# Kernel tuning notes

Hardware: AMD Instinct MI355X
Metric: run time of the kernel (lower is better)

Reference implementation:

```python
import jax, jax.numpy as jnp
import numpy as np

NS, NF, D = 50000, 100000, 128
E1, E2 = 600000, 600000


def setup_inputs() -> dict:
    key = jax.random.key(0)
    ks = jax.random.split(key, 9)
    return {
        "h_station": jax.random.normal(ks[0], (NS, D), dtype=jnp.float32),
        "h_feature": jax.random.normal(ks[1], (NF, D), dtype=jnp.float32),
        "Wself": jax.random.normal(ks[2], (3, 2, D, D), dtype=jnp.float32) * (1.0 / np.sqrt(D)),
        "Wneigh": jax.random.normal(ks[3], (3, 2, D, D), dtype=jnp.float32) * (1.0 / np.sqrt(D)),
        "bias": jnp.zeros((3, 2, D), dtype=jnp.float32),
        "hf_src": jax.random.randint(ks[4], (E1,), 0, NF, dtype=jnp.int32),
        "hf_dst": jax.random.randint(ks[5], (E1,), 0, NS, dtype=jnp.int32),
        "tt_src": jax.random.randint(ks[6], (E2,), 0, NS, dtype=jnp.int32),
        "tt_dst": jax.random.randint(ks[7], (E2,), 0, NS, dtype=jnp.int32),
    }


def _mean_agg(h_src, src, dst, n_dst):
    # gather source features along edges, segment-mean into destinations
    msgs = h_src[src]  # [E, D]
    s = jax.ops.segment_sum(msgs, dst, num_segments=n_dst)
    deg = jax.ops.segment_sum(jnp.ones((src.shape[0], 1), h_src.dtype), dst, num_segments=n_dst)
    return s / jnp.maximum(deg, 1.0)  # zero-in-degree nodes -> 0 (DGL behavior)


def _sage(h_dst, neigh, Ws, Wn, b):
    # DGL SAGEConv (mean): act(fc_self(h_dst) + fc_neigh(neigh) + bias)
    return jax.nn.relu(h_dst @ Ws + neigh @ Wn + b)


def reference(h_station, h_feature, Wself, Wneigh, bias, hf_src, hf_dst, tt_src, tt_dst):
    ns = h_station.shape[0]
    # --- layer 1: HeteroGraphConv aggregate='sum' over both relations (dst='station')
    n_hf = _mean_agg(h_feature, hf_src, hf_dst, ns)
    n_tt = _mean_agg(h_station, tt_src, tt_dst, ns)
    out_hf = _sage(h_station, n_hf, Wself[0, 0], Wneigh[0, 0], bias[0, 0])
    out_tt = _sage(h_station, n_tt, Wself[0, 1], Wneigh[0, 1], bias[0, 1])
    h = out_hf + out_tt
    # --- layers 2,3: 'feature' repr no longer present -> HAS_FEATURE relation skipped
    for l in (1, 2):
        n_tt = _mean_agg(h, tt_src, tt_dst, ns)
        h = _sage(h, n_tt, Wself[l, 1], Wneigh[l, 1], bias[l, 1])
    return h
```

## Files before the change

kernel.cpp:

```cpp
#include <hip/hip_runtime.h>

#define D 128
#define NBIN 256
#define K1_EPB 4096
#define BCAP 6144

typedef __attribute__((ext_vector_type(8)))  short s16x8;
typedef __attribute__((ext_vector_type(4)))  short s16x4;
typedef __attribute__((ext_vector_type(16))) float f32x16;

static __device__ __forceinline__ unsigned short f2bf(float x) {
    unsigned u = __builtin_bit_cast(unsigned, x);
    unsigned r = (u + 0x7FFF + ((u >> 16) & 1)) >> 16;
    return (unsigned short)r;
}
static __device__ __forceinline__ float bf2f(unsigned short h) {
    unsigned u = ((unsigned)h) << 16;
    return __builtin_bit_cast(float, u);
}
static __device__ __forceinline__ float bflo(unsigned v) {
    return __builtin_bit_cast(float, v << 16);
}
static __device__ __forceinline__ float bfhi(unsigned v) {
    return __builtin_bit_cast(float, v & 0xFFFF0000u);
}


__global__ __launch_bounds__(256) void convert_kernel(
    const float* __restrict__ h_station, unsigned short* __restrict__ st_h,
    int ns_elem, int nbs,
    const float* __restrict__ h_feature, unsigned short* __restrict__ feat_h,
    int nf_elem, int nbf,
    const float* __restrict__ Wself, const float* __restrict__ Wneigh,
    short* __restrict__ wt)
{
    int b = blockIdx.x;
    int tid = threadIdx.x;
    if (b < nbs) {
        int i = (b * 256 + tid) * 4;
        if (i < ns_elem) {
            float4 v = *(const float4*)(h_station + i);
            s16x4 hv;
            hv[0] = (short)f2bf(v.x);
            hv[1] = (short)f2bf(v.y);
            hv[2] = (short)f2bf(v.z);
            hv[3] = (short)f2bf(v.w);
            *(s16x4*)(st_h + i) = hv;
        }
        return;
    }
    b -= nbs;
    if (b < nbf) {
        int i = (b * 256 + tid) * 4;
        if (i < nf_elem) {
            float4 v = *(const float4*)(h_feature + i);
            s16x4 hv;
            hv[0] = (short)f2bf(v.x);
            hv[1] = (short)f2bf(v.y);
            hv[2] = (short)f2bf(v.z);
            hv[3] = (short)f2bf(v.w);
            *(s16x4*)(feat_h + i) = hv;
        }
        return;
    }
    b -= nbf;
    {
        int g = b * 256 + tid;
        int m = g >> 11;
        int e = g & 2047;
        int n  = e >> 4;
        int kg = e & 15;
        int kk0 = kg >> 3;
        int kl0 = (kg & 7) * 8;
        int pair = m >> 1, s = m & 1;
        int l = (pair == 3) ? 2 : ((pair == 2) ? 1 : 0);
        int r = (pair == 0) ? 0 : 1;
        const float* W = (s ? Wneigh : Wself) + (size_t)(l * 2 + r) * D * D;
        s16x8 hv;
        #pragma unroll
        for (int c = 0; c < 8; ++c) {
            int k = kk0 * 64 + kl0 + c;
            hv[c] = (short)f2bf(W[(size_t)k * D + n]);
        }
        int ksb = kl0 ^ ((n & 7) << 3);
        size_t base = ((size_t)(pair * 2 + s) * 2 + kk0) * 8192;
        *(s16x8*)&wt[base + n * 64 + ksb] = hv;
    }
}


__global__ __launch_bounds__(256) void hist_rank_kernel(
    const int* __restrict__ dst1, int E1, int nblk1, int* __restrict__ hist1,
    unsigned short* __restrict__ rank1,
    const int* __restrict__ dst2, int E2, int nblk2, int* __restrict__ hist2,
    unsigned short* __restrict__ rank2)
{
    __shared__ int h[NBIN];
    int b = blockIdx.x;
    const int* dst; int E, nblk; int* hist; unsigned short* rank;
    if (b < nblk1) { dst = dst1; E = E1; nblk = nblk1; hist = hist1; rank = rank1; }
    else { b -= nblk1; dst = dst2; E = E2; nblk = nblk2; hist = hist2; rank = rank2; }
    int t = threadIdx.x;
    h[t] = 0;
    __syncthreads();
    int base = b * K1_EPB;
    #pragma unroll 1
    for (int j = 0; j < 16; ++j) {
        int i = base + j * 256 + t;
        if (i < E) {
            int bin = dst[i] >> 8;
            int r = atomicAdd(&h[bin], 1);
            rank[i] = (unsigned short)r;
        }
    }
    __syncthreads();
    hist[t * nblk + b] = h[t];
}

__global__ __launch_bounds__(256) void scan_blocks_g(
    const int* __restrict__ in1, int* __restrict__ out1, int* __restrict__ bs1, int L1,
    const int* __restrict__ in2, int* __restrict__ out2, int* __restrict__ bs2, int L2,
    int nb1)
{
    int gid = blockIdx.x;
    const int* in; int* out; int* bs; int b; int L;
    if (gid < nb1) { in = in1; out = out1; bs = bs1; b = gid; L = L1; }
    else          { in = in2; out = out2; bs = bs2; b = gid - nb1; L = L2; }
    int t = threadIdx.x;
    int i0 = b * 1024 + t * 4;
    int4 v = make_int4(0, 0, 0, 0);
    if (i0 + 3 < L) v = *(const int4*)(in + i0);
    else {
        if (i0 + 0 < L) v.x = in[i0 + 0];
        if (i0 + 1 < L) v.y = in[i0 + 1];
        if (i0 + 2 < L) v.z = in[i0 + 2];
        if (i0 + 3 < L) v.w = in[i0 + 3];
    }
    __shared__ int sm[256];
    sm[t] = v.x + v.y + v.z + v.w;
    __syncthreads();
    for (int off = 1; off < 256; off <<= 1) {
        int x = (t >= off) ? sm[t - off] : 0;
        __syncthreads();
        sm[t] += x;
        __syncthreads();
    }
    int excl = (t > 0) ? sm[t - 1] : 0;
    if (i0 + 0 < L) out[i0 + 0] = excl;
    if (i0 + 1 < L) out[i0 + 1] = excl + v.x;
    if (i0 + 2 < L) out[i0 + 2] = excl + v.x + v.y;
    if (i0 + 3 < L) out[i0 + 3] = excl + v.x + v.y + v.z;
    if (t == 255) bs[b] = sm[255];
}

__global__ __launch_bounds__(256) void scan_offsets_g(
    int* __restrict__ out1, const int* __restrict__ bs1, int L1,
    int* __restrict__ out2, const int* __restrict__ bs2, int L2, int nb1)
{
    int gid = blockIdx.x;
    int* out; const int* bs; int b; int L;
    if (gid < nb1) { out = out1; bs = bs1; b = gid; L = L1; }
    else          { out = out2; bs = bs2; b = gid - nb1; L = L2; }
    int t = threadIdx.x;
    int lane = t & 63;
    int partial = 0;
    for (int i = lane; i < b; i += 64) partial += bs[i];
    #pragma unroll
    for (int off = 32; off; off >>= 1) partial += __shfl_xor(partial, off);
    if (partial == 0) return;
    int i0 = b * 1024 + t * 4;
    if (i0 + 0 < L) out[i0 + 0] += partial;
    if (i0 + 1 < L) out[i0 + 1] += partial;
    if (i0 + 2 < L) out[i0 + 2] += partial;
    if (i0 + 3 < L) out[i0 + 3] += partial;
}

__global__ __launch_bounds__(256) void scatter_kernel(
    const int* __restrict__ dst1, const int* __restrict__ src1,
    const unsigned short* __restrict__ rank1, const int* __restrict__ off1,
    unsigned* __restrict__ bkt1, int E1, int nblk1,
    const int* __restrict__ dst2, const int* __restrict__ src2,
    const unsigned short* __restrict__ rank2, const int* __restrict__ off2,
    unsigned* __restrict__ bkt2, int E2, int nblk2)
{
    int b = blockIdx.x;
    const int* dst; const int* src; const unsigned short* rank; const int* off;
    unsigned* bkt; int E, nblk;
    if (b < nblk1) { dst = dst1; src = src1; rank = rank1; off = off1; bkt = bkt1; E = E1; nblk = nblk1; }
    else { b -= nblk1; dst = dst2; src = src2; rank = rank2; off = off2; bkt = bkt2; E = E2; nblk = nblk2; }
    int t = threadIdx.x;
    int base = b * K1_EPB;
    #pragma unroll 1
    for (int j = 0; j < 16; ++j) {
        int i = base + j * 256 + t;
        if (i < E) {
            int d = dst[i];
            int bin = d >> 8;
            int pos = off[bin * nblk + b] + rank[i];
            bkt[pos] = ((unsigned)(d & 255) << 24) | (unsigned)src[i];
        }
    }
}

__global__ __launch_bounds__(256) void bucket_csr_kernel(
    const unsigned* __restrict__ bkt1, const int* __restrict__ off1, int E1, int nblk1,
    int* __restrict__ col1, int* __restrict__ rp1,
    const unsigned* __restrict__ bkt2, const int* __restrict__ off2, int E2, int nblk2,
    int* __restrict__ col2, int* __restrict__ rp2, int NSn)
{
    __shared__ int h[NBIN];
    __shared__ int pre[NBIN];
    __shared__ int cur[NBIN];
    __shared__ int colbuf[BCAP];
    int bin = blockIdx.x;
    const unsigned* bkt; const int* off; int E, nblk; int* col; int* rp;
    if (bin < NBIN) { bkt = bkt1; off = off1; E = E1; nblk = nblk1; col = col1; rp = rp1; }
    else { bin -= NBIN; bkt = bkt2; off = off2; E = E2; nblk = nblk2; col = col2; rp = rp2; }
    int t = threadIdx.x;
    int start = off[bin * nblk];
    int end = (bin == NBIN - 1) ? E : off[(bin + 1) * nblk];
    int n = end - start;

    h[t] = 0;
    __syncthreads();
    for (int p = t; p < n; p += 256) atomicAdd(&h[bkt[start + p] >> 24], 1);
    __syncthreads();
    int hv = h[t];
    pre[t] = hv;
    __syncthreads();
    for (int o = 1; o < 256; o <<= 1) {
        int x = (t >= o) ? pre[t - o] : 0;
        __syncthreads();
        pre[t] += x;
        __syncthreads();
    }
    int excl = pre[t] - hv;
    cur[t] = excl;
    __syncthreads();
    for (int p = t; p < n; p += 256) {
        unsigned v = bkt[start + p];
        int lo = v >> 24;
        int pos = atomicAdd(&cur[lo], 1);
        if (pos < BCAP) colbuf[pos] = (int)(v & 0xFFFFFF);
    }
    __syncthreads();
    for (int p = t; p < n; p += 256) col[start + p] = colbuf[p];
    int dstid = bin * 256 + t;
    if (dstid < NSn) rp[dstid] = start + excl;
    if (bin == 0 && t == 0) rp[NSn] = E;
}


static __device__ __forceinline__ void agg_body(
    const unsigned short* __restrict__ hsrc, const int* __restrict__ rowptr,
    const int* __restrict__ col, unsigned short* __restrict__ oh,
    int row4, int ndst, int lane)
{
    const int q  = lane >> 4;
    const int ql = lane & 15;
    const int row = row4 + q;
    const bool valid = row < ndst;
    int beg = 0, end = 0;
    if (valid) { beg = rowptr[row]; end = rowptr[row + 1]; }
    int deg = end - beg;

    float a0 = 0.f, a1 = 0.f, a2 = 0.f, a3 = 0.f;
    float a4 = 0.f, a5 = 0.f, a6 = 0.f, a7 = 0.f;
    const unsigned short* base = hsrc + ql * 8;

    for (int b = beg; b < end; b += 16) {
        int n = min(16, end - b);
        int myidx = (ql < n) ? col[b + ql] : 0;
        int j = 0;
        for (; j + 2 <= n; j += 2) {
            int s0 = __shfl(myidx, (q << 4) + j);
            int s1 = __shfl(myidx, (q << 4) + j + 1);
            uint4 v0 = *(const uint4*)(base + (size_t)s0 * D);
            uint4 v1 = *(const uint4*)(base + (size_t)s1 * D);
            a0 += bflo(v0.x); a1 += bfhi(v0.x);
            a2 += bflo(v0.y); a3 += bfhi(v0.y);
            a4 += bflo(v0.z); a5 += bfhi(v0.z);
            a6 += bflo(v0.w); a7 += bfhi(v0.w);
            a0 += bflo(v1.x); a1 += bfhi(v1.x);
            a2 += bflo(v1.y); a3 += bfhi(v1.y);
            a4 += bflo(v1.z); a5 += bfhi(v1.z);
            a6 += bflo(v1.w); a7 += bfhi(v1.w);
        }
        if (j < n) {
            int s0 = __shfl(myidx, (q << 4) + j);
            uint4 v0 = *(const uint4*)(base + (size_t)s0 * D);
            a0 += bflo(v0.x); a1 += bfhi(v0.x);
            a2 += bflo(v0.y); a3 += bfhi(v0.y);
            a4 += bflo(v0.z); a5 += bfhi(v0.z);
            a6 += bflo(v0.w); a7 += bfhi(v0.w);
        }
    }
    if (valid) {
        float inv = 1.0f / fmaxf((float)deg, 1.0f);
        s16x8 o;
        o[0] = (short)f2bf(a0 * inv);
        o[1] = (short)f2bf(a1 * inv);
        o[2] = (short)f2bf(a2 * inv);
        o[3] = (short)f2bf(a3 * inv);
        o[4] = (short)f2bf(a4 * inv);
        o[5] = (short)f2bf(a5 * inv);
        o[6] = (short)f2bf(a6 * inv);
        o[7] = (short)f2bf(a7 * inv);
        *(s16x8*)(oh + (size_t)row * D + ql * 8) = o;
    }
}

__global__ __launch_bounds__(256) void agg_mean_kernel(
    const unsigned short* __restrict__ hsrc, const int* __restrict__ rowptr,
    const int* __restrict__ col, unsigned short* __restrict__ oh, int ndst) {
    int wave = (blockIdx.x * blockDim.x + threadIdx.x) >> 6;
    int row4 = wave * 4;
    if (row4 >= ndst) return;
    agg_body(hsrc, rowptr, col, oh, row4, ndst, threadIdx.x & 63);
}

__global__ __launch_bounds__(256) void agg_l1_kernel(
    const unsigned short* __restrict__ feat, const int* __restrict__ rp_hf,
    const int* __restrict__ col_hf, unsigned short* __restrict__ n1,
    const unsigned short* __restrict__ st, const int* __restrict__ rp_tt,
    const int* __restrict__ col_tt, unsigned short* __restrict__ n2,
    int ndst, int gsplit)
{
    int b = blockIdx.x;
    if (b < gsplit) {
        int row4 = ((b * 256 + threadIdx.x) >> 6) * 4;
        if (row4 >= ndst) return;
        agg_body(feat, rp_hf, col_hf, n1, row4, ndst, threadIdx.x & 63);
    } else {
        int row4 = (((b - gsplit) * 256 + threadIdx.x) >> 6) * 4;
        if (row4 >= ndst) return;
        agg_body(st, rp_tt, col_tt, n2, row4, ndst, threadIdx.x & 63);
    }
}


template<bool ACC, bool WF32>
__global__ __launch_bounds__(256) void sage_gemm_kernel(
    const unsigned short* __restrict__ Ah_g, const unsigned short* __restrict__ Nh_g,
    const short* __restrict__ wtp, const float* __restrict__ bias,
    float* __restrict__ Yf, unsigned short* __restrict__ Yh, int M)
{
    __shared__ short lds[16384];
    short* AhS = lds;
    short* BhS = lds + 4096;

    const int tid = threadIdx.x;
    const int l = tid & 63, w = tid >> 6;
    const int wr = w >> 1, wc = w & 1;
    const int row0 = blockIdx.x * 64;

    f32x16 acc[2] = {};

    const int s_row = tid >> 2;
    const int s_k   = (tid & 3) * 16;
    const int s_sw  = (s_row & 7) << 3;
    const int arow  = wr * 32 + (l & 31);
    const int fsw   = (l & 7) << 3;
    const int afk   = (l >> 5) * 8;

    #pragma unroll 1
    for (int st = 0; st < 4; ++st) {
        const unsigned short* Hg = (st < 2) ? Ah_g : Nh_g;
        const unsigned short* hrow = Hg + (size_t)(row0 + s_row) * D + (st & 1) * 64 + s_k;
        s16x8 a0 = *(const s16x8*)(hrow);
        s16x8 a1 = *(const s16x8*)(hrow + 8);
        const short* wsrc = wtp + (size_t)st * 8192;
        s16x8 b0 = *(const s16x8*)(wsrc + tid * 8);
        s16x8 b1 = *(const s16x8*)(wsrc + 2048 + tid * 8);
        s16x8 b2 = *(const s16x8*)(wsrc + 4096 + tid * 8);
        s16x8 b3 = *(const s16x8*)(wsrc + 6144 + tid * 8);
        __syncthreads();
        *(s16x8*)&AhS[s_row * 64 + (s_k ^ s_sw)]       = a0;
        *(s16x8*)&AhS[s_row * 64 + ((s_k + 8) ^ s_sw)] = a1;
        *(s16x8*)&BhS[tid * 8]        = b0;
        *(s16x8*)&BhS[2048 + tid * 8] = b1;
        *(s16x8*)&BhS[4096 + tid * 8] = b2;
        *(s16x8*)&BhS[6144 + tid * 8] = b3;
        __syncthreads();
        #pragma unroll
        for (int kc = 0; kc < 4; ++kc) {
            int ak = (kc * 16 + afk) ^ fsw;
            s16x8 ah = *(const s16x8*)&AhS[arow * 64 + ak];
            #pragma unroll
            for (int nt = 0; nt < 2; ++nt) {
                int brow = wc * 64 + nt * 32 + (l & 31);
                s16x8 bh = *(const s16x8*)&BhS[brow * 64 + ak];
                acc[nt] = __builtin_amdgcn_mfma_f32_32x32x16_bf16(ah, bh, acc[nt], 0, 0, 0);
            }
        }
    }

    __syncthreads();
    float* fstage = (float*)lds;
    const int colb = l & 31;
    const int rq4  = (l >> 5) * 4;
    #pragma unroll
    for (int nt = 0; nt < 2; ++nt) {
        int col = wc * 64 + nt * 32 + colb;
        float bias_c = bias[col];
        #pragma unroll
        for (int g = 0; g < 4; ++g) {
            #pragma unroll
            for (int q = 0; q < 4; ++q) {
                int r = wr * 32 + q + g * 8 + rq4;
                fstage[r * 128 + col] = fmaxf(acc[nt][g * 4 + q] + bias_c, 0.f);
            }
        }
    }
    __syncthreads();
    int orow = tid >> 2;
    int ocol = (tid & 3) * 32;
    int grow = row0 + orow;
    if (grow < M) {
        size_t base = (size_t)grow * D + ocol;
        float vals[32];
        #pragma unroll
        for (int c = 0; c < 32; c += 4)
            *(float4*)&vals[c] = *(const float4*)&fstage[orow * 128 + ocol + c];
        if (ACC) {
            #pragma unroll
            for (int c8 = 0; c8 < 4; ++c8) {
                s16x8 oh = *(const s16x8*)(Yh + base + c8 * 8);
                #pragma unroll
                for (int e = 0; e < 8; ++e)
                    vals[c8 * 8 + e] += bf2f((unsigned short)oh[e]);
            }
        }
        if (WF32) {
            #pragma unroll
            for (int c = 0; c < 32; c += 4)
                *(float4*)(Yf + base + c) = *(const float4*)&vals[c];
        } else {
            #pragma unroll
            for (int c8 = 0; c8 < 4; ++c8) {
                s16x8 hv;
                #pragma unroll
                for (int e = 0; e < 8; ++e)
                    hv[e] = (short)f2bf(vals[c8 * 8 + e]);
                *(s16x8*)(Yh + base + c8 * 8) = hv;
            }
        }
    }
}


extern "C" void kernel_launch(void* const* d_in, const int* in_sizes, int n_in,
                              void* d_out, int out_size, void* d_ws, size_t ws_size,
                              hipStream_t stream) {
    const float* h_station = (const float*)d_in[0];
    const float* h_feature = (const float*)d_in[1];
    const float* Wself     = (const float*)d_in[2];
    const float* Wneigh    = (const float*)d_in[3];
    const float* bias      = (const float*)d_in[4];
    const int* hf_src = (const int*)d_in[5];
    const int* hf_dst = (const int*)d_in[6];
    const int* tt_src = (const int*)d_in[7];
    const int* tt_dst = (const int*)d_in[8];

    const int NS = in_sizes[0] / D;
    const int NF = in_sizes[1] / D;
    const int E1 = in_sizes[5];
    const int E2 = in_sizes[7];
    const int NSP = (NS + 63) & ~63;

    char* ws = (char*)d_ws;
    size_t off = 0;
    auto alloc = [&](size_t bytes) -> void* {
        void* p = ws + off;
        off = (off + bytes + 255) & ~(size_t)255;
        return p;
    };
    unsigned short* st_h  = (unsigned short*)alloc((size_t)NSP * D * 2);
    unsigned short* n_h   = (unsigned short*)alloc((size_t)NSP * D * 2);
    unsigned short* n_h2  = (unsigned short*)alloc((size_t)NSP * D * 2);
    unsigned short* hbreg = (unsigned short*)alloc((size_t)2 * NSP * D * 2);
    unsigned short* hb_h  = hbreg;
    int* rp_hf    = (int*)alloc((size_t)(NS + 1) * sizeof(int));
    int* col_hf   = (int*)alloc((size_t)E1 * sizeof(int));
    int* rp_tt    = (int*)alloc((size_t)(NS + 1) * sizeof(int));
    int* col_tt   = (int*)alloc((size_t)E2 * sizeof(int));
    short* wt     = (short*)alloc((size_t)4 * 32768 * sizeof(short));

    const int nblk1 = (E1 + K1_EPB - 1) / K1_EPB;
    const int nblk2 = (E2 + K1_EPB - 1) / K1_EPB;
    const int L1 = NBIN * nblk1;
    const int L2 = NBIN * nblk2;
    int* hist1 = (int*)alloc((size_t)L1 * sizeof(int));
    int* hist2 = (int*)alloc((size_t)L2 * sizeof(int));
    int* off1  = (int*)alloc((size_t)L1 * sizeof(int));
    int* off2  = (int*)alloc((size_t)L2 * sizeof(int));
    unsigned short* rank1 = (unsigned short*)alloc((size_t)E1 * 2);
    unsigned short* rank2 = (unsigned short*)alloc((size_t)E2 * 2);
    unsigned* bkt1 = (unsigned*)alloc((size_t)E1 * sizeof(unsigned));
    unsigned* bkt2 = (unsigned*)alloc((size_t)E2 * sizeof(unsigned));
    const int nbs1 = (L1 + 1023) / 1024;
    const int nbs2 = (L2 + 1023) / 1024;
    int* bsA = (int*)alloc((size_t)nbs1 * sizeof(int));
    int* bsB = (int*)alloc((size_t)nbs2 * sizeof(int));

    unsigned short* feat_h = hbreg;

    const int tpb = 256;
    int nbs = (NS * D / 4 + tpb - 1) / tpb;
    int nbf = (NF * D / 4 + tpb - 1) / tpb;

    convert_kernel<<<nbs + nbf + 64, tpb, 0, stream>>>(
        h_station, st_h, NS * D, nbs, h_feature, feat_h, NF * D, nbf,
        Wself, Wneigh, wt);
    hist_rank_kernel<<<nblk1 + nblk2, tpb, 0, stream>>>(
        hf_dst, E1, nblk1, hist1, rank1, tt_dst, E2, nblk2, hist2, rank2);
    scan_blocks_g<<<nbs1 + nbs2, tpb, 0, stream>>>(
        hist1, off1, bsA, L1, hist2, off2, bsB, L2, nbs1);
    scan_offsets_g<<<nbs1 + nbs2, tpb, 0, stream>>>(
        off1, bsA, L1, off2, bsB, L2, nbs1);
    scatter_kernel<<<nblk1 + nblk2, tpb, 0, stream>>>(
        hf_dst, hf_src, rank1, off1, bkt1, E1, nblk1,
        tt_dst, tt_src, rank2, off2, bkt2, E2, nblk2);
    bucket_csr_kernel<<<2 * NBIN, tpb, 0, stream>>>(
        bkt1, off1, E1, nblk1, col_hf, rp_hf,
        bkt2, off2, E2, nblk2, col_tt, rp_tt, NS);

    int gagg  = (NS + 15) / 16;
    int ggemm = NSP / 64;

    auto BI = [&](int lidx, int r) { return bias + (size_t)(lidx * 2 + r) * D; };
    auto WT = [&](int pair) { return wt + (size_t)pair * 32768; };

    float* out = (float*)d_out;

    agg_l1_kernel<<<2 * gagg, tpb, 0, stream>>>(feat_h, rp_hf, col_hf, n_h,
                                                st_h, rp_tt, col_tt, n_h2, NS, gagg);
    sage_gemm_kernel<false, false><<<ggemm, tpb, 0, stream>>>(
        st_h, n_h, WT(0), BI(0,0), nullptr, hb_h, NS);
    sage_gemm_kernel<true, false><<<ggemm, tpb, 0, stream>>>(
        st_h, n_h2, WT(1), BI(0,1), nullptr, hb_h, NS);

    agg_mean_kernel<<<gagg, tpb, 0, stream>>>(hb_h, rp_tt, col_tt, n_h, NS);
    sage_gemm_kernel<false, false><<<ggemm, tpb, 0, stream>>>(
        hb_h, n_h, WT(2), BI(1,1), nullptr, hb_h, NS);

    agg_mean_kernel<<<gagg, tpb, 0, stream>>>(hb_h, rp_tt, col_tt, n_h, NS);
    sage_gemm_kernel<false, true><<<ggemm, tpb, 0, stream>>>(
        hb_h, n_h, WT(3), BI(2,1), out, nullptr, NS);
}
```

Baseline: 209.5 us.

## Fuse mean aggregation into SAGE GEMM for layers 2-3 and merge prep kernels

Layers 2 and 3 now run as one kernel each. Every block gathers the neighbour mean for its 64 rows into LDS and then runs the self and neighbour GEMM in place, so the intermediate neighbour tensor no longer makes a round trip through global memory and a launch is saved. Ping-pong output buffers are introduced because the fused kernel reads neighbour rows written by other blocks. The histogram/rank kernel is also merged into the conversion kernel, removing one more launch. The cost is that each GEMM block is serialised behind its gather phase, and the larger LDS footprint may lower occupancy.

```diff
diff --git a/kernel.cpp b/kernel.cpp
--- a/kernel.cpp
+++ b/kernel.cpp
@@ -26,7 +26,11 @@
 }
 
 
-__global__ __launch_bounds__(256) void convert_kernel(
+__global__ __launch_bounds__(256) void pre_kernel(
+    const int* __restrict__ dst1, int E1, int nblk1, int* __restrict__ hist1,
+    unsigned short* __restrict__ rank1,
+    const int* __restrict__ dst2, int E2, int nblk2, int* __restrict__ hist2,
+    unsigned short* __restrict__ rank2,
     const float* __restrict__ h_station, unsigned short* __restrict__ st_h,
     int ns_elem, int nbs,
     const float* __restrict__ h_feature, unsigned short* __restrict__ feat_h,
@@ -34,10 +38,32 @@
     const float* __restrict__ Wself, const float* __restrict__ Wneigh,
     short* __restrict__ wt)
 {
+    __shared__ int h[NBIN];
     int b = blockIdx.x;
-    int tid = threadIdx.x;
+    int t = threadIdx.x;
+    if (b < nblk1 + nblk2) {
+        const int* dst; int E, nblk; int* hist; unsigned short* rank;
+        if (b < nblk1) { dst = dst1; E = E1; nblk = nblk1; hist = hist1; rank = rank1; }
+        else { b -= nblk1; dst = dst2; E = E2; nblk = nblk2; hist = hist2; rank = rank2; }
+        h[t] = 0;
+        __syncthreads();
+        int base = b * K1_EPB;
+        #pragma unroll 1
+        for (int j = 0; j < 16; ++j) {
+            int i = base + j * 256 + t;
+            if (i < E) {
+                int bin = dst[i] >> 8;
+                int r = atomicAdd(&h[bin], 1);
+                rank[i] = (unsigned short)r;
+            }
+        }
+        __syncthreads();
+        hist[t * nblk + b] = h[t];
+        return;
+    }
+    b -= nblk1 + nblk2;
     if (b < nbs) {
-        int i = (b * 256 + tid) * 4;
+        int i = (b * 256 + t) * 4;
         if (i < ns_elem) {
             float4 v = *(const float4*)(h_station + i);
             s16x4 hv;
@@ -51,7 +77,7 @@
     }
     b -= nbs;
     if (b < nbf) {
-        int i = (b * 256 + tid) * 4;
+        int i = (b * 256 + t) * 4;
         if (i < nf_elem) {
             float4 v = *(const float4*)(h_feature + i);
             s16x4 hv;
@@ -65,7 +91,7 @@
     }
     b -= nbf;
     {
-        int g = b * 256 + tid;
+        int g = b * 256 + t;
         int m = g >> 11;
         int e = g & 2047;
         int n  = e >> 4;
@@ -88,34 +114,6 @@
     }
 }
 
-
-__global__ __launch_bounds__(256) void hist_rank_kernel(
-    const int* __restrict__ dst1, int E1, int nblk1, int* __restrict__ hist1,
-    unsigned short* __restrict__ rank1,
-    const int* __restrict__ dst2, int E2, int nblk2, int* __restrict__ hist2,
-    unsigned short* __restrict__ rank2)
-{
-    __shared__ int h[NBIN];
-    int b = blockIdx.x;
-    const int* dst; int E, nblk; int* hist; unsigned short* rank;
-    if (b < nblk1) { dst = dst1; E = E1; nblk = nblk1; hist = hist1; rank = rank1; }
-    else { b -= nblk1; dst = dst2; E = E2; nblk = nblk2; hist = hist2; rank = rank2; }
-    int t = threadIdx.x;
-    h[t] = 0;
-    __syncthreads();
-    int base = b * K1_EPB;
-    #pragma unroll 1
-    for (int j = 0; j < 16; ++j) {
-        int i = base + j * 256 + t;
-        if (i < E) {
-            int bin = dst[i] >> 8;
-            int r = atomicAdd(&h[bin], 1);
-            rank[i] = (unsigned short)r;
-        }
-    }
-    __syncthreads();
-    hist[t * nblk + b] = h[t];
-}
 
 __global__ __launch_bounds__(256) void scan_blocks_g(
     const int* __restrict__ in1, int* __restrict__ out1, int* __restrict__ bs1, int L1,
@@ -310,15 +308,6 @@
     }
 }
 
-__global__ __launch_bounds__(256) void agg_mean_kernel(
-    const unsigned short* __restrict__ hsrc, const int* __restrict__ rowptr,
-    const int* __restrict__ col, unsigned short* __restrict__ oh, int ndst) {
-    int wave = (blockIdx.x * blockDim.x + threadIdx.x) >> 6;
-    int row4 = wave * 4;
-    if (row4 >= ndst) return;
-    agg_body(hsrc, rowptr, col, oh, row4, ndst, threadIdx.x & 63);
-}
-
 __global__ __launch_bounds__(256) void agg_l1_kernel(
     const unsigned short* __restrict__ feat, const int* __restrict__ rp_hf,
     const int* __restrict__ col_hf, unsigned short* __restrict__ n1,
@@ -339,11 +328,11 @@
 }
 
 
-template<bool ACC, bool WF32>
+template<bool ACC>
 __global__ __launch_bounds__(256) void sage_gemm_kernel(
     const unsigned short* __restrict__ Ah_g, const unsigned short* __restrict__ Nh_g,
     const short* __restrict__ wtp, const float* __restrict__ bias,
-    float* __restrict__ Yf, unsigned short* __restrict__ Yh, int M)
+    unsigned short* __restrict__ Yh, int M)
 {
     __shared__ short lds[16384];
     short* AhS = lds;
@@ -431,17 +420,172 @@
                     vals[c8 * 8 + e] += bf2f((unsigned short)oh[e]);
             }
         }
+        #pragma unroll
+        for (int c8 = 0; c8 < 4; ++c8) {
+            s16x8 hv;
+            #pragma unroll
+            for (int e = 0; e < 8; ++e)
+                hv[e] = (short)f2bf(vals[c8 * 8 + e]);
+            *(s16x8*)(Yh + base + c8 * 8) = hv;
+        }
+    }
+}
+
+
+template<bool WF32>
+__global__ __launch_bounds__(256) void fused_layer_kernel(
+    const unsigned short* __restrict__ Hg,
+    const int* __restrict__ rowptr, const int* __restrict__ col,
+    const short* __restrict__ wtp, const float* __restrict__ bias,
+    float* __restrict__ Yf, unsigned short* __restrict__ Yh, int M)
+{
+    __shared__ short lds[20480];
+    short* NhS = lds;
+    short* AhS = lds + 8192;
+    short* BhS = lds + 12288;
+
+    const int tid = threadIdx.x;
+    const int l = tid & 63, w = tid >> 6;
+    const int wr = w >> 1, wc = w & 1;
+    const int row0 = blockIdx.x * 64;
+
+    {
+        const int q  = l >> 4;
+        const int ql = l & 15;
+        const unsigned short* base = Hg + ql * 8;
+        #pragma unroll 1
+        for (int it = 0; it < 4; ++it) {
+            int lrow = w * 16 + it * 4 + q;
+            int row = row0 + lrow;
+            int beg = 0, end = 0;
+            if (row < M) { beg = rowptr[row]; end = rowptr[row + 1]; }
+            int deg = end - beg;
+            float a0 = 0.f, a1 = 0.f, a2 = 0.f, a3 = 0.f;
+            float a4 = 0.f, a5 = 0.f, a6 = 0.f, a7 = 0.f;
+            for (int b = beg; b < end; b += 16) {
+                int n = min(16, end - b);
+                int myidx = (ql < n) ? col[b + ql] : 0;
+                int j = 0;
+                for (; j + 2 <= n; j += 2) {
+                    int s0 = __shfl(myidx, (q << 4) + j);
+                    int s1 = __shfl(myidx, (q << 4) + j + 1);
+                    uint4 v0 = *(const uint4*)(base + (size_t)s0 * D);
+                    uint4 v1 = *(const uint4*)(base + (size_t)s1 * D);
+                    a0 += bflo(v0.x); a1 += bfhi(v0.x);
+                    a2 += bflo(v0.y); a3 += bfhi(v0.y);
+                    a4 += bflo(v0.z); a5 += bfhi(v0.z);
+                    a6 += bflo(v0.w); a7 += bfhi(v0.w);
+                    a0 += bflo(v1.x); a1 += bfhi(v1.x);
+                    a2 += bflo(v1.y); a3 += bfhi(v1.y);
+                    a4 += bflo(v1.z); a5 += bfhi(v1.z);
+                    a6 += bflo(v1.w); a7 += bfhi(v1.w);
+                }
+                if (j < n) {
+                    int s0 = __shfl(myidx, (q << 4) + j);
+                    uint4 v0 = *(const uint4*)(base + (size_t)s0 * D);
+                    a0 += bflo(v0.x); a1 += bfhi(v0.x);
+                    a2 += bflo(v0.y); a3 += bfhi(v0.y);
+                    a4 += bflo(v0.z); a5 += bfhi(v0.z);
+                    a6 += bflo(v0.w); a7 += bfhi(v0.w);
+                }
+            }
+            float inv = 1.0f / fmaxf((float)deg, 1.0f);
+            s16x8 o;
+            o[0] = (short)f2bf(a0 * inv);
+            o[1] = (short)f2bf(a1 * inv);
+            o[2] = (short)f2bf(a2 * inv);
+            o[3] = (short)f2bf(a3 * inv);
+            o[4] = (short)f2bf(a4 * inv);
+            o[5] = (short)f2bf(a5 * inv);
+            o[6] = (short)f2bf(a6 * inv);
+            o[7] = (short)f2bf(a7 * inv);
+            int sw = (lrow & 7) << 3;
+            *(s16x8*)&NhS[lrow * 128 + (ql >> 3) * 64 + (((ql & 7) * 8) ^ sw)] = o;
+        }
+    }
+
+    f32x16 acc[2] = {};
+    const int s_row = tid >> 2;
+    const int s_k   = (tid & 3) * 16;
+    const int s_sw  = (s_row & 7) << 3;
+    const int arow  = wr * 32 + (l & 31);
+    const int fsw   = (l & 7) << 3;
+    const int afk   = (l >> 5) * 8;
+
+    #pragma unroll 1
+    for (int st = 0; st < 4; ++st) {
+        bool selfst = (st < 2);
+        s16x8 a0, a1;
+        if (selfst) {
+            const unsigned short* hrow = Hg + (size_t)(row0 + s_row) * D + (st & 1) * 64 + s_k;
+            a0 = *(const s16x8*)(hrow);
+            a1 = *(const s16x8*)(hrow + 8);
+        }
+        const short* wsrc = wtp + (size_t)st * 8192;
+        s16x8 b0 = *(const s16x8*)(wsrc + tid * 8);
+        s16x8 b1 = *(const s16x8*)(wsrc + 2048 + tid * 8);
+        s16x8 b2 = *(const s16x8*)(wsrc + 4096 + tid * 8);
+        s16x8 b3 = *(const s16x8*)(wsrc + 6144 + tid * 8);
+        __syncthreads();
+        if (selfst) {
+            *(s16x8*)&AhS[s_row * 64 + (s_k ^ s_sw)]       = a0;
+            *(s16x8*)&AhS[s_row * 64 + ((s_k + 8) ^ s_sw)] = a1;
+        }
+        *(s16x8*)&BhS[tid * 8]        = b0;
+        *(s16x8*)&BhS[2048 + tid * 8] = b1;
+        *(s16x8*)&BhS[4096 + tid * 8] = b2;
+        *(s16x8*)&BhS[6144 + tid * 8] = b3;
+        __syncthreads();
+        #pragma unroll
+        for (int kc = 0; kc < 4; ++kc) {
+            int ak = (kc * 16 + afk) ^ fsw;
+            s16x8 ah = selfst ? *(const s16x8*)&AhS[arow * 64 + ak]
+                              : *(const s16x8*)&NhS[arow * 128 + (st & 1) * 64 + ak];
+            #pragma unroll
+            for (int nt = 0; nt < 2; ++nt) {
+                int brow = wc * 64 + nt * 32 + (l & 31);
+                s16x8 bh = *(const s16x8*)&BhS[brow * 64 + ak];
+                acc[nt] = __builtin_amdgcn_mfma_f32_32x32x16_bf16(ah, bh, acc[nt], 0, 0, 0);
+            }
+        }
+    }
+
+    __syncthreads();
+    float* fstage = (float*)lds;
+    const int colb = l & 31;
+    const int rq4  = (l >> 5) * 4;
+    #pragma unroll
+    for (int nt = 0; nt < 2; ++nt) {
+        int col2 = wc * 64 + nt * 32 + colb;
+        float bias_c = bias[col2];
+        #pragma unroll
+        for (int g = 0; g < 4; ++g) {
+            #pragma unroll
+            for (int q = 0; q < 4; ++q) {
+                int r = wr * 32 + q + g * 8 + rq4;
+                fstage[r * 128 + col2] = fmaxf(acc[nt][g * 4 + q] + bias_c, 0.f);
+            }
+        }
+    }
+    __syncthreads();
+    int orow = tid >> 2;
+    int ocol = (tid & 3) * 32;
+    int grow = row0 + orow;
+    if (grow < M) {
+        size_t base = (size_t)grow * D + ocol;
         if (WF32) {
             #pragma unroll
-            for (int c = 0; c < 32; c += 4)
-                *(float4*)(Yf + base + c) = *(const float4*)&vals[c];
+            for (int c = 0; c < 32; c += 4) {
+                float4 v = *(const float4*)&fstage[orow * 128 + ocol + c];
+                *(float4*)(Yf + base + c) = v;
+            }
         } else {
             #pragma unroll
             for (int c8 = 0; c8 < 4; ++c8) {
                 s16x8 hv;
                 #pragma unroll
                 for (int e = 0; e < 8; ++e)
-                    hv[e] = (short)f2bf(vals[c8 * 8 + e]);
+                    hv[e] = (short)f2bf(fstage[orow * 128 + ocol + c8 * 8 + e]);
                 *(s16x8*)(Yh + base + c8 * 8) = hv;
             }
         }
@@ -479,7 +623,8 @@
     unsigned short* n_h   = (unsigned short*)alloc((size_t)NSP * D * 2);
     unsigned short* n_h2  = (unsigned short*)alloc((size_t)NSP * D * 2);
     unsigned short* hbreg = (unsigned short*)alloc((size_t)2 * NSP * D * 2);
-    unsigned short* hb_h  = hbreg;
+    unsigned short* hb0   = hbreg;
+    unsigned short* hb1   = hbreg + (size_t)NSP * D;
     int* rp_hf    = (int*)alloc((size_t)(NS + 1) * sizeof(int));
     int* col_hf   = (int*)alloc((size_t)E1 * sizeof(int));
     int* rp_tt    = (int*)alloc((size_t)(NS + 1) * sizeof(int));
@@ -509,11 +654,10 @@
     int nbs = (NS * D / 4 + tpb - 1) / tpb;
     int nbf = (NF * D / 4 + tpb - 1) / tpb;
 
-    convert_kernel<<<nbs + nbf + 64, tpb, 0, stream>>>(
+    pre_kernel<<<nblk1 + nblk2 + nbs + nbf + 64, tpb, 0, stream>>>(
+        hf_dst, E1, nblk1, hist1, rank1, tt_dst, E2, nblk2, hist2, rank2,
         h_station, st_h, NS * D, nbs, h_feature, feat_h, NF * D, nbf,
         Wself, Wneigh, wt);
-    hist_rank_kernel<<<nblk1 + nblk2, tpb, 0, stream>>>(
-        hf_dst, E1, nblk1, hist1, rank1, tt_dst, E2, nblk2, hist2, rank2);
     scan_blocks_g<<<nbs1 + nbs2, tpb, 0, stream>>>(
         hist1, off1, bsA, L1, hist2, off2, bsB, L2, nbs1);
     scan_offsets_g<<<nbs1 + nbs2, tpb, 0, stream>>>(
@@ -535,16 +679,14 @@
 
     agg_l1_kernel<<<2 * gagg, tpb, 0, stream>>>(feat_h, rp_hf, col_hf, n_h,
                                                 st_h, rp_tt, col_tt, n_h2, NS, gagg);
-    sage_gemm_kernel<false, false><<<ggemm, tpb, 0, stream>>>(
-        st_h, n_h, WT(0), BI(0,0), nullptr, hb_h, NS);
-    sage_gemm_kernel<true, false><<<ggemm, tpb, 0, stream>>>(
-        st_h, n_h2, WT(1), BI(0,1), nullptr, hb_h, NS);
-
-    agg_mean_kernel<<<gagg, tpb, 0, stream>>>(hb_h, rp_tt, col_tt, n_h, NS);
-    sage_gemm_kernel<false, false><<<ggemm, tpb, 0, stream>>>(
-        hb_h, n_h, WT(2), BI(1,1), nullptr, hb_h, NS);
-
-    agg_mean_kernel<<<gagg, tpb, 0, stream>>>(hb_h, rp_tt, col_tt, n_h, NS);
-    sage_gemm_kernel<false, true><<<ggemm, tpb, 0, stream>>>(
-        hb_h, n_h, WT(3), BI(2,1), out, nullptr, NS);
-}
+    sage_gemm_kernel<false><<<ggemm, tpb, 0, stream>>>(
+        st_h, n_h, WT(0), BI(0,0), hb0, NS);
+    sage_gemm_kernel<true><<<ggemm, tpb, 0, stream>>>(
+        st_h, n_h2, WT(1), BI(0,1), hb0, NS);
+
+    fused_layer_kernel<false><<<ggemm, tpb, 0, stream>>>(
+        hb0, rp_tt, col_tt, WT(2), BI(1,1), nullptr, hb1, NS);
+
+    fused_layer_kernel<true><<<ggemm, tpb, 0, stream>>>(
+        hb1, rp_tt, col_tt, WT(3), BI(2,1), out, nullptr, NS);
+}
```

After: 197.8 us. 5.6% less time.

## Fuse mean aggregation into SAGE GEMM kernel and merge histogram into convert

Applied to the files above, without the earlier changes.

Each layer's neighbor mean aggregation is now computed inside the GEMM kernel. Every block gathers its 64 destination rows into LDS, so the aggregated neighbor tensor never round-trips through global memory, and the separate aggregation launches disappear. Layers 2 and 3 now ping-pong between two output buffers instead of writing in place. The histogram/rank pass is also merged into the conversion kernel to save a launch. The trade-off is that the gather now runs on only NSP/64 blocks with 4 waves each, which may reduce latency hiding, and LDS use per block grows.

```diff
diff --git a/kernel.cpp b/kernel.cpp
--- a/kernel.cpp
+++ b/kernel.cpp
@@ -26,7 +26,11 @@
 }
 
 
-__global__ __launch_bounds__(256) void convert_kernel(
+__global__ __launch_bounds__(256) void pre_kernel(
+    const int* __restrict__ dst1, int E1, int nblk1, int* __restrict__ hist1,
+    unsigned short* __restrict__ rank1,
+    const int* __restrict__ dst2, int E2, int nblk2, int* __restrict__ hist2,
+    unsigned short* __restrict__ rank2,
     const float* __restrict__ h_station, unsigned short* __restrict__ st_h,
     int ns_elem, int nbs,
     const float* __restrict__ h_feature, unsigned short* __restrict__ feat_h,
@@ -34,10 +38,32 @@
     const float* __restrict__ Wself, const float* __restrict__ Wneigh,
     short* __restrict__ wt)
 {
+    __shared__ int h[NBIN];
     int b = blockIdx.x;
-    int tid = threadIdx.x;
+    int t = threadIdx.x;
+    if (b < nblk1 + nblk2) {
+        const int* dst; int E, nblk; int* hist; unsigned short* rank;
+        if (b < nblk1) { dst = dst1; E = E1; nblk = nblk1; hist = hist1; rank = rank1; }
+        else { b -= nblk1; dst = dst2; E = E2; nblk = nblk2; hist = hist2; rank = rank2; }
+        h[t] = 0;
+        __syncthreads();
+        int base = b * K1_EPB;
+        #pragma unroll 1
+        for (int j = 0; j < 16; ++j) {
+            int i = base + j * 256 + t;
+            if (i < E) {
+                int bin = dst[i] >> 8;
+                int r = atomicAdd(&h[bin], 1);
+                rank[i] = (unsigned short)r;
+            }
+        }
+        __syncthreads();
+        hist[t * nblk + b] = h[t];
+        return;
+    }
+    b -= nblk1 + nblk2;
     if (b < nbs) {
-        int i = (b * 256 + tid) * 4;
+        int i = (b * 256 + t) * 4;
         if (i < ns_elem) {
             float4 v = *(const float4*)(h_station + i);
             s16x4 hv;
@@ -51,7 +77,7 @@
     }
     b -= nbs;
     if (b < nbf) {
-        int i = (b * 256 + tid) * 4;
+        int i = (b * 256 + t) * 4;
         if (i < nf_elem) {
             float4 v = *(const float4*)(h_feature + i);
             s16x4 hv;
@@ -65,7 +91,7 @@
     }
     b -= nbf;
     {
-        int g = b * 256 + tid;
+        int g = b * 256 + t;
         int m = g >> 11;
         int e = g & 2047;
         int n  = e >> 4;
@@ -88,34 +114,6 @@
     }
 }
 
-
-__global__ __launch_bounds__(256) void hist_rank_kernel(
-    const int* __restrict__ dst1, int E1, int nblk1, int* __restrict__ hist1,
-    unsigned short* __restrict__ rank1,
-    const int* __restrict__ dst2, int E2, int nblk2, int* __restrict__ hist2,
-    unsigned short* __restrict__ rank2)
-{
-    __shared__ int h[NBIN];
-    int b = blockIdx.x;
-    const int* dst; int E, nblk; int* hist; unsigned short* rank;
-    if (b < nblk1) { dst = dst1; E = E1; nblk = nblk1; hist = hist1; rank = rank1; }
-    else { b -= nblk1; dst = dst2; E = E2; nblk = nblk2; hist = hist2; rank = rank2; }
-    int t = threadIdx.x;
-    h[t] = 0;
-    __syncthreads();
-    int base = b * K1_EPB;
-    #pragma unroll 1
-    for (int j = 0; j < 16; ++j) {
-        int i = base + j * 256 + t;
-        if (i < E) {
-            int bin = dst[i] >> 8;
-            int r = atomicAdd(&h[bin], 1);
-            rank[i] = (unsigned short)r;
-        }
-    }
-    __syncthreads();
-    hist[t * nblk + b] = h[t];
-}
 
 __global__ __launch_bounds__(256) void scan_blocks_g(
     const int* __restrict__ in1, int* __restrict__ out1, int* __restrict__ bs1, int L1,
@@ -251,111 +249,80 @@
 }
 
 
-static __device__ __forceinline__ void agg_body(
-    const unsigned short* __restrict__ hsrc, const int* __restrict__ rowptr,
-    const int* __restrict__ col, unsigned short* __restrict__ oh,
-    int row4, int ndst, int lane)
-{
-    const int q  = lane >> 4;
-    const int ql = lane & 15;
-    const int row = row4 + q;
-    const bool valid = row < ndst;
-    int beg = 0, end = 0;
-    if (valid) { beg = rowptr[row]; end = rowptr[row + 1]; }
-    int deg = end - beg;
-
-    float a0 = 0.f, a1 = 0.f, a2 = 0.f, a3 = 0.f;
-    float a4 = 0.f, a5 = 0.f, a6 = 0.f, a7 = 0.f;
-    const unsigned short* base = hsrc + ql * 8;
-
-    for (int b = beg; b < end; b += 16) {
-        int n = min(16, end - b);
-        int myidx = (ql < n) ? col[b + ql] : 0;
-        int j = 0;
-        for (; j + 2 <= n; j += 2) {
-            int s0 = __shfl(myidx, (q << 4) + j);
-            int s1 = __shfl(myidx, (q << 4) + j + 1);
-            uint4 v0 = *(const uint4*)(base + (size_t)s0 * D);
-            uint4 v1 = *(const uint4*)(base + (size_t)s1 * D);
-            a0 += bflo(v0.x); a1 += bfhi(v0.x);
-            a2 += bflo(v0.y); a3 += bfhi(v0.y);
-            a4 += bflo(v0.z); a5 += bfhi(v0.z);
-            a6 += bflo(v0.w); a7 += bfhi(v0.w);
-            a0 += bflo(v1.x); a1 += bfhi(v1.x);
-            a2 += bflo(v1.y); a3 += bfhi(v1.y);
-            a4 += bflo(v1.z); a5 += bfhi(v1.z);
-            a6 += bflo(v1.w); a7 += bfhi(v1.w);
-        }
-        if (j < n) {
-            int s0 = __shfl(myidx, (q << 4) + j);
-            uint4 v0 = *(const uint4*)(base + (size_t)s0 * D);
-            a0 += bflo(v0.x); a1 += bfhi(v0.x);
-            a2 += bflo(v0.y); a3 += bfhi(v0.y);
-            a4 += bflo(v0.z); a5 += bfhi(v0.z);
-            a6 += bflo(v0.w); a7 += bfhi(v0.w);
-        }
-    }
-    if (valid) {
-        float inv = 1.0f / fmaxf((float)deg, 1.0f);
-        s16x8 o;
-        o[0] = (short)f2bf(a0 * inv);
-        o[1] = (short)f2bf(a1 * inv);
-        o[2] = (short)f2bf(a2 * inv);
-        o[3] = (short)f2bf(a3 * inv);
-        o[4] = (short)f2bf(a4 * inv);
-        o[5] = (short)f2bf(a5 * inv);
-        o[6] = (short)f2bf(a6 * inv);
-        o[7] = (short)f2bf(a7 * inv);
-        *(s16x8*)(oh + (size_t)row * D + ql * 8) = o;
-    }
-}
-
-__global__ __launch_bounds__(256) void agg_mean_kernel(
-    const unsigned short* __restrict__ hsrc, const int* __restrict__ rowptr,
-    const int* __restrict__ col, unsigned short* __restrict__ oh, int ndst) {
-    int wave = (blockIdx.x * blockDim.x + threadIdx.x) >> 6;
-    int row4 = wave * 4;
-    if (row4 >= ndst) return;
-    agg_body(hsrc, rowptr, col, oh, row4, ndst, threadIdx.x & 63);
-}
-
-__global__ __launch_bounds__(256) void agg_l1_kernel(
-    const unsigned short* __restrict__ feat, const int* __restrict__ rp_hf,
-    const int* __restrict__ col_hf, unsigned short* __restrict__ n1,
-    const unsigned short* __restrict__ st, const int* __restrict__ rp_tt,
-    const int* __restrict__ col_tt, unsigned short* __restrict__ n2,
-    int ndst, int gsplit)
-{
-    int b = blockIdx.x;
-    if (b < gsplit) {
-        int row4 = ((b * 256 + threadIdx.x) >> 6) * 4;
-        if (row4 >= ndst) return;
-        agg_body(feat, rp_hf, col_hf, n1, row4, ndst, threadIdx.x & 63);
-    } else {
-        int row4 = (((b - gsplit) * 256 + threadIdx.x) >> 6) * 4;
-        if (row4 >= ndst) return;
-        agg_body(st, rp_tt, col_tt, n2, row4, ndst, threadIdx.x & 63);
-    }
-}
-
-
 template<bool ACC, bool WF32>
-__global__ __launch_bounds__(256) void sage_gemm_kernel(
-    const unsigned short* __restrict__ Ah_g, const unsigned short* __restrict__ Nh_g,
+__global__ __launch_bounds__(256) void fused_layer_kernel(
+    const unsigned short* __restrict__ Sg,
+    const unsigned short* __restrict__ Gg,
+    const int* __restrict__ rowptr, const int* __restrict__ col,
     const short* __restrict__ wtp, const float* __restrict__ bias,
     float* __restrict__ Yf, unsigned short* __restrict__ Yh, int M)
 {
-    __shared__ short lds[16384];
-    short* AhS = lds;
-    short* BhS = lds + 4096;
+    __shared__ short lds[20480];
+    short* NhS = lds;
+    short* AhS = lds + 8192;
+    short* BhS = lds + 12288;
 
     const int tid = threadIdx.x;
     const int l = tid & 63, w = tid >> 6;
     const int wr = w >> 1, wc = w & 1;
     const int row0 = blockIdx.x * 64;
 
+    {
+        const int q  = l >> 4;
+        const int ql = l & 15;
+        const unsigned short* base = Gg + ql * 8;
+        #pragma unroll 1
+        for (int it = 0; it < 4; ++it) {
+            int lrow = w * 16 + it * 4 + q;
+            int row = row0 + lrow;
+            int beg = 0, end = 0;
+            if (row < M) { beg = rowptr[row]; end = rowptr[row + 1]; }
+            int deg = end - beg;
+            float a0 = 0.f, a1 = 0.f, a2 = 0.f, a3 = 0.f;
+            float a4 = 0.f, a5 = 0.f, a6 = 0.f, a7 = 0.f;
+            for (int b = beg; b < end; b += 16) {
+                int n = min(16, end - b);
+                int myidx = (ql < n) ? col[b + ql] : 0;
+                int j = 0;
+                for (; j + 2 <= n; j += 2) {
+                    int s0 = __shfl(myidx, (q << 4) + j);
+                    int s1 = __shfl(myidx, (q << 4) + j + 1);
+                    uint4 v0 = *(const uint4*)(base + (size_t)s0 * D);
+                    uint4 v1 = *(const uint4*)(base + (size_t)s1 * D);
+                    a0 += bflo(v0.x); a1 += bfhi(v0.x);
+                    a2 += bflo(v0.y); a3 += bfhi(v0.y);
+                    a4 += bflo(v0.z); a5 += bfhi(v0.z);
+                    a6 += bflo(v0.w); a7 += bfhi(v0.w);
+                    a0 += bflo(v1.x); a1 += bfhi(v1.x);
+                    a2 += bflo(v1.y); a3 += bfhi(v1.y);
+                    a4 += bflo(v1.z); a5 += bfhi(v1.z);
+                    a6 += bflo(v1.w); a7 += bfhi(v1.w);
+                }
+                if (j < n) {
+                    int s0 = __shfl(myidx, (q << 4) + j);
+                    uint4 v0 = *(const uint4*)(base + (size_t)s0 * D);
+                    a0 += bflo(v0.x); a1 += bfhi(v0.x);
+                    a2 += bflo(v0.y); a3 += bfhi(v0.y);
+                    a4 += bflo(v0.z); a5 += bfhi(v0.z);
+                    a6 += bflo(v0.w); a7 += bfhi(v0.w);
+                }
+            }
+            float inv = 1.0f / fmaxf((float)deg, 1.0f);
+            s16x8 o;
+            o[0] = (short)f2bf(a0 * inv);
+            o[1] = (short)f2bf(a1 * inv);
+            o[2] = (short)f2bf(a2 * inv);
+            o[3] = (short)f2bf(a3 * inv);
+            o[4] = (short)f2bf(a4 * inv);
+            o[5] = (short)f2bf(a5 * inv);
+            o[6] = (short)f2bf(a6 * inv);
+            o[7] = (short)f2bf(a7 * inv);
+            int sw = (lrow & 7) << 3;
+            *(s16x8*)&NhS[lrow * 128 + (ql >> 3) * 64 + (((ql & 7) * 8) ^ sw)] = o;
+        }
+    }
+
     f32x16 acc[2] = {};
-
     const int s_row = tid >> 2;
     const int s_k   = (tid & 3) * 16;
     const int s_sw  = (s_row & 7) << 3;
@@ -365,18 +332,23 @@
 
     #pragma unroll 1
     for (int st = 0; st < 4; ++st) {
-        const unsigned short* Hg = (st < 2) ? Ah_g : Nh_g;
-        const unsigned short* hrow = Hg + (size_t)(row0 + s_row) * D + (st & 1) * 64 + s_k;
-        s16x8 a0 = *(const s16x8*)(hrow);
-        s16x8 a1 = *(const s16x8*)(hrow + 8);
+        bool selfst = (st < 2);
+        s16x8 a0, a1;
+        if (selfst) {
+            const unsigned short* hrow = Sg + (size_t)(row0 + s_row) * D + (st & 1) * 64 + s_k;
+            a0 = *(const s16x8*)(hrow);
+            a1 = *(const s16x8*)(hrow + 8);
+        }
         const short* wsrc = wtp + (size_t)st * 8192;
         s16x8 b0 = *(const s16x8*)(wsrc + tid * 8);
         s16x8 b1 = *(const s16x8*)(wsrc + 2048 + tid * 8);
         s16x8 b2 = *(const s16x8*)(wsrc + 4096 + tid * 8);
         s16x8 b3 = *(const s16x8*)(wsrc + 6144 + tid * 8);
         __syncthreads();
-        *(s16x8*)&AhS[s_row * 64 + (s_k ^ s_sw)]       = a0;
-        *(s16x8*)&AhS[s_row * 64 + ((s_k + 8) ^ s_sw)] = a1;
+        if (selfst) {
+            *(s16x8*)&AhS[s_row * 64 + (s_k ^ s_sw)]       = a0;
+            *(s16x8*)&AhS[s_row * 64 + ((s_k + 8) ^ s_sw)] = a1;
+        }
         *(s16x8*)&BhS[tid * 8]        = b0;
         *(s16x8*)&BhS[2048 + tid * 8] = b1;
         *(s16x8*)&BhS[4096 + tid * 8] = b2;
@@ -385,7 +357,8 @@
         #pragma unroll
         for (int kc = 0; kc < 4; ++kc) {
             int ak = (kc * 16 + afk) ^ fsw;
-            s16x8 ah = *(const s16x8*)&AhS[arow * 64 + ak];
+            s16x8 ah = selfst ? *(const s16x8*)&AhS[arow * 64 + ak]
+                              : *(const s16x8*)&NhS[arow * 128 + (st & 1) * 64 + ak];
             #pragma unroll
             for (int nt = 0; nt < 2; ++nt) {
                 int brow = wc * 64 + nt * 32 + (l & 31);
@@ -401,14 +374,14 @@
     const int rq4  = (l >> 5) * 4;
     #pragma unroll
     for (int nt = 0; nt < 2; ++nt) {
-        int col = wc * 64 + nt * 32 + colb;
-        float bias_c = bias[col];
+        int col2 = wc * 64 + nt * 32 + colb;
+        float bias_c = bias[col2];
         #pragma unroll
         for (int g = 0; g < 4; ++g) {
             #pragma unroll
             for (int q = 0; q < 4; ++q) {
                 int r = wr * 32 + q + g * 8 + rq4;
-                fstage[r * 128 + col] = fmaxf(acc[nt][g * 4 + q] + bias_c, 0.f);
+                fstage[r * 128 + col2] = fmaxf(acc[nt][g * 4 + q] + bias_c, 0.f);
             }
         }
     }
@@ -479,7 +452,8 @@
     unsigned short* n_h   = (unsigned short*)alloc((size_t)NSP * D * 2);
     unsigned short* n_h2  = (unsigned short*)alloc((size_t)NSP * D * 2);
     unsigned short* hbreg = (unsigned short*)alloc((size_t)2 * NSP * D * 2);
-    unsigned short* hb_h  = hbreg;
+    unsigned short* hb0   = hbreg;
+    unsigned short* hb1   = hbreg + (size_t)NSP * D;
     int* rp_hf    = (int*)alloc((size_t)(NS + 1) * sizeof(int));
     int* col_hf   = (int*)alloc((size_t)E1 * sizeof(int));
     int* rp_tt    = (int*)alloc((size_t)(NS + 1) * sizeof(int));
@@ -503,17 +477,16 @@
     int* bsA = (int*)alloc((size_t)nbs1 * sizeof(int));
     int* bsB = (int*)alloc((size_t)nbs2 * sizeof(int));
 
-    unsigned short* feat_h = hbreg;
+    unsigned short* feat_h = n_h;
 
     const int tpb = 256;
     int nbs = (NS * D / 4 + tpb - 1) / tpb;
     int nbf = (NF * D / 4 + tpb - 1) / tpb;
 
-    convert_kernel<<<nbs + nbf + 64, tpb, 0, stream>>>(
+    pre_kernel<<<nblk1 + nblk2 + nbs + nbf + 64, tpb, 0, stream>>>(
+        hf_dst, E1, nblk1, hist1, rank1, tt_dst, E2, nblk2, hist2, rank2,
         h_station, st_h, NS * D, nbs, h_feature, feat_h, NF * D, nbf,
         Wself, Wneigh, wt);
-    hist_rank_kernel<<<nblk1 + nblk2, tpb, 0, stream>>>(
-        hf_dst, E1, nblk1, hist1, rank1, tt_dst, E2, nblk2, hist2, rank2);
     scan_blocks_g<<<nbs1 + nbs2, tpb, 0, stream>>>(
         hist1, off1, bsA, L1, hist2, off2, bsB, L2, nbs1);
     scan_offsets_g<<<nbs1 + nbs2, tpb, 0, stream>>>(
@@ -525,26 +498,17 @@
         bkt1, off1, E1, nblk1, col_hf, rp_hf,
         bkt2, off2, E2, nblk2, col_tt, rp_tt, NS);
 
-    int gagg  = (NS + 15) / 16;
     int ggemm = NSP / 64;
-
     auto BI = [&](int lidx, int r) { return bias + (size_t)(lidx * 2 + r) * D; };
     auto WT = [&](int pair) { return wt + (size_t)pair * 32768; };
-
     float* out = (float*)d_out;
 
-    agg_l1_kernel<<<2 * gagg, tpb, 0, stream>>>(feat_h, rp_hf, col_hf, n_h,
-                                                st_h, rp_tt, col_tt, n_h2, NS, gagg);
-    sage_gemm_kernel<false, false><<<ggemm, tpb, 0, stream>>>(
-        st_h, n_h, WT(0), BI(0,0), nullptr, hb_h, NS);
-    sage_gemm_kernel<true, false><<<ggemm, tpb, 0, stream>>>(
-        st_h, n_h2, WT(1), BI(0,1), nullptr, hb_h, NS);
-
-    agg_mean_kernel<<<gagg, tpb, 0, stream>>>(hb_h, rp_tt, col_tt, n_h, NS);
-    sage_gemm_kernel<false, false><<<ggemm, tpb, 0, stream>>>(
-        hb_h, n_h, WT(2), BI(1,1), nullptr, hb_h, NS);
-
-    agg_mean_kernel<<<gagg, tpb, 0, stream>>>(hb_h, rp_tt, col_tt, n_h, NS);
-    sage_gemm_kernel<false, true><<<ggemm, tpb, 0, stream>>>(
-        hb_h, n_h, WT(3), BI(2,1), out, nullptr, NS);
-}
+    fused_layer_kernel<false, false><<<ggemm, tpb, 0, stream>>>(
+        st_h, feat_h, rp_hf, col_hf, WT(0), BI(0,0), nullptr, hb0, NS);
+    fused_layer_kernel<true, false><<<ggemm, tpb, 0, stream>>>(
+        st_h, st_h, rp_tt, col_tt, WT(1), BI(0,1), nullptr, hb0, NS);
+    fused_layer_kernel<false, false><<<ggemm, tpb, 0, stream>>>(
+        hb0, hb0, rp_tt, col_tt, WT(2), BI(1,1), nullptr, hb1, NS);
+    fused_layer_kernel<false, true><<<ggemm, tpb, 0, stream>>>(
+        hb1, hb1, rp_tt, col_tt, WT(3), BI(2,1), out, nullptr, NS);
+}
```

Result: faster. 196.3 us (-6.3%).
